# Kernel tuning notes

Hardware: AMD Instinct MI355X
Metric: run time of the kernel (lower is better)

## Reference

```python
import jax, jax.numpy as jnp
import numpy as np
import math

NUM_FILTERS = 128
SAMPLE_RATE = 16000
N_FFT = 2048
FREQ_MIN, FREQ_MAX = 20.0, 8000.0


def setup_inputs() -> dict:
    key = jax.random.key(0)
    B, FB, T = 32, N_FFT // 2 + 1, 2000
    spectrum = jax.random.normal(key, (B, FB, T), dtype=jnp.float32)
    # mel-scale init of center frequencies (in FFT-bin units), as in __init__
    mel_min = 2595.0 * math.log10(1.0 + FREQ_MIN / 700.0)
    mel_max = 2595.0 * math.log10(1.0 + FREQ_MAX / 700.0)
    mel_points = jnp.linspace(mel_min, mel_max, NUM_FILTERS, dtype=jnp.float32)
    freq_points = 700.0 * (10.0 ** (mel_points / 2595.0) - 1.0)
    center_freqs = freq_points * N_FFT / SAMPLE_RATE  # [F]
    bandwidths = jnp.full((NUM_FILTERS,), N_FFT / NUM_FILTERS / 4.0, dtype=jnp.float32)
    filter_shapes = jnp.ones((NUM_FILTERS, 2), dtype=jnp.float32)
    return {"spectrum": spectrum, "center_freqs": center_freqs,
            "bandwidths": bandwidths, "filter_shapes": filter_shapes}


def _build_filterbank(center_freqs, bandwidths, filter_shapes, freq_bins):
    # Vectorized over all filters: [F, freq_bins]
    freqs = jnp.arange(freq_bins, dtype=jnp.float32)[None, :]        # [1, K]
    center = center_freqs[:, None]                                    # [F, 1]
    bw = (jax.nn.softplus(bandwidths) + 0.001)[:, None]               # [F, 1]
    slopes = jax.nn.softplus(filter_shapes) + 0.1                     # [F, 2]
    left_edge = center - bw * slopes[:, 0:1]
    right_edge = center + bw * slopes[:, 1:2]
    rise = (freqs >= left_edge) & (freqs <= center)
    fall = (freqs > center) & (freqs <= right_edge)
    resp = jnp.where(rise, (freqs - left_edge) / (center - left_edge + 1e-8), 0.0)
    resp = jnp.where(fall, 1.0 - (freqs - center) / (right_edge - center + 1e-8), resp)
    return resp  # [F, K]


def reference(spectrum, center_freqs, bandwidths, filter_shapes):
    B, K, T = spectrum.shape
    F = center_freqs.shape[0]
    filterbank = _build_filterbank(center_freqs, bandwidths, filter_shapes, K)
    # [F, K] x [B, K, T] -> [B, F, T]
    filtered = jnp.einsum('fk,bkt->bft', filterbank, spectrum)
    # Faithful to original: reshape [B, F, T] -> [F, B, T], then permute(1,2,0) -> [B, T, F]
    filtered = filtered.reshape(F, B, T)
    return jnp.transpose(filtered, (1, 2, 0))
```

## Files before the change

kernel.cpp:

```cpp
#include <hip/hip_runtime.h>

#define K_BINS 1025
#define T_LEN  2000
#define NF     128
#define TQ     500
#define ROWQ   500
#define SLICE  524

__device__ __forceinline__ float softplusf(float x) {
    return fmaxf(x, 0.0f) + log1pf(expf(-fabsf(x)));
}

__global__ __launch_bounds__(1024) void fb_fused(
        const float* __restrict__ spec,
        const float* __restrict__ cf,
        const float* __restrict__ bwv,
        const float* __restrict__ fs,
        float*       __restrict__ out) {
    __shared__ float tile2[16][4 * SLICE];

    const int q    = blockIdx.x;
    const int B    = blockIdx.y;
    const int th   = blockIdx.z;
    const int tid  = threadIdx.x;
    const int lane = tid & 63;
    const int wid  = tid >> 6;
    const int w    = wid >> 2;
    const int p    = wid & 3;
    const int bp   = 4 * q + p;
    const int t0   = TQ * th;
    const bool ok1 = lane < (TQ / 4 - 64);
    const int  li1 = min(64 + lane, TQ / 4 - 1);

    const float4* base4 =
        (const float4*)(spec + (size_t)bp * (K_BINS * (size_t)T_LEN) + t0);

    float ic[4], mir[4], mA[4], Bfc[4];
    int   klo4[4], khi4[4];
#pragma unroll
    for (int i = 0; i < 4; ++i) {
        const int f = 4 * B + 32 * w + i;
        float c  = cf[f];
        float bw = softplusf(bwv[f]) + 0.001f;
        float s0 = softplusf(fs[2 * f])     + 0.1f;
        float s1 = softplusf(fs[2 * f + 1]) + 0.1f;
        float left  = c - bw * s0;
        float right = c + bw * s1;
        float icv = 1.0f / (c - left + 1e-8f);
        float irv = 1.0f / (right - c + 1e-8f);
        ic[i]  = icv;
        mir[i] = -irv;
        mA[i]  = -left * icv;
        Bfc[i] = fmaf(c, irv, 1.0f);
        klo4[i] = max(0, (int)ceilf(left));
        khi4[i] = min(K_BINS - 1, (int)floorf(right));
    }

    int RS0 = klo4[0], RE0 = khi4[0];
    int RS1 = 0, RE1 = -1, RS2 = 0, RE2 = -1, RS3 = 0, RE3 = -1;
    int nr = 1;
#pragma unroll
    for (int i = 1; i < 4; ++i) {
        const int s = klo4[i], e = khi4[i];
        const int le = (nr == 1) ? RE0 : (nr == 2) ? RE1 : RE2;
        if (s <= le + 1) {
            const int ne = max(le, e);
            if (nr == 1) RE0 = ne; else if (nr == 2) RE1 = ne; else RE2 = ne;
        } else {
            if (nr == 1)      { RS1 = s; RE1 = e; }
            else if (nr == 2) { RS2 = s; RE2 = e; }
            else              { RS3 = s; RE3 = e; }
            ++nr;
        }
    }

    float4 acc[4][2];
#pragma unroll
    for (int i = 0; i < 4; ++i) {
        acc[i][0] = make_float4(0.f, 0.f, 0.f, 0.f);
        acc[i][1] = make_float4(0.f, 0.f, 0.f, 0.f);
    }

#define ROWSTEP(KK, VA, VB)                                                 \
    { const int   k_  = (KK);                                               \
      const float fk_ = (float)k_;                                          \
      const bool  lv_ = (k_ <= ke);      \
      _Pragma("unroll")                                                     \
      for (int i = 0; i < 4; ++i) {                                         \
          float wg = fmaxf(0.0f, fminf(fmaf(fk_, ic[i],  mA[i]),            \
                                       fmaf(fk_, mir[i], Bfc[i])));         \
          wg = lv_ ? wg : 0.0f;                                             \
          acc[i][0].x = fmaf(wg, VA.x, acc[i][0].x);                        \
          acc[i][0].y = fmaf(wg, VA.y, acc[i][0].y);                        \
          acc[i][0].z = fmaf(wg, VA.z, acc[i][0].z);                        \
          acc[i][0].w = fmaf(wg, VA.w, acc[i][0].w);                        \
          acc[i][1].x = fmaf(wg, VB.x, acc[i][1].x);                        \
          acc[i][1].y = fmaf(wg, VB.y, acc[i][1].y);                        \
          acc[i][1].z = fmaf(wg, VB.z, acc[i][1].z);                        \
          acc[i][1].w = fmaf(wg, VB.w, acc[i][1].w);                        \
      } }

#pragma unroll
    for (int r = 0; r < 4; ++r) {
        int ks, ke;
        if      (r == 0) { ks = RS0; ke = RE0; }
        else if (r == 1) { ks = RS1; ke = RE1; }
        else if (r == 2) { ks = RS2; ke = RE2; }
        else             { ks = RS3; ke = RE3; }
        for (int k0 = ks; k0 <= ke; k0 += 4) {
            const float4* rp0 = base4 + (size_t)min(k0,     K_BINS - 1) * ROWQ;
            const float4* rp1 = base4 + (size_t)min(k0 + 1, K_BINS - 1) * ROWQ;
            const float4* rp2 = base4 + (size_t)min(k0 + 2, K_BINS - 1) * ROWQ;
            const float4* rp3 = base4 + (size_t)min(k0 + 3, K_BINS - 1) * ROWQ;
            float4 a0 = rp0[lane], b0 = rp0[li1];
            float4 a1 = rp1[lane], b1 = rp1[li1];
            float4 a2 = rp2[lane], b2 = rp2[li1];
            float4 a3 = rp3[lane], b3 = rp3[li1];
            ROWSTEP(k0 + 0, a0, b0);
            ROWSTEP(k0 + 1, a1, b1);
            ROWSTEP(k0 + 2, a2, b2);
            ROWSTEP(k0 + 3, a3, b3);
        }
    }
#undef ROWSTEP

    {
        const int col = 4 * p + w;
#pragma unroll
        for (int i = 0; i < 4; ++i) {
            *reinterpret_cast<float4*>(&tile2[col][i * SLICE + 4 * lane]) = acc[i][0];
            if (ok1)
                *reinterpret_cast<float4*>(&tile2[col][i * SLICE + 256 + 4 * lane]) = acc[i][1];
        }
    }
    __syncthreads();
    {
        const int c4 = tid & 3;
#pragma unroll
        for (int i = 0; i < 4; ++i) {
            const int b2 = 4 * B + i;
#pragma unroll
            for (int rr = 0; rr < 2; ++rr) {
                int tl = 256 * rr + (tid >> 2);
                if (tl < TQ) {
                    float4 v = make_float4(tile2[4 * c4 + 0][i * SLICE + tl],
                                           tile2[4 * c4 + 1][i * SLICE + tl],
                                           tile2[4 * c4 + 2][i * SLICE + tl],
                                           tile2[4 * c4 + 3][i * SLICE + tl]);
                    *reinterpret_cast<float4*>(
                        out + ((size_t)b2 * T_LEN + t0 + tl) * NF + 16 * q + 4 * c4) = v;
                }
            }
        }
    }
}

extern "C" void kernel_launch(void* const* d_in, const int* in_sizes, int n_in,
                              void* d_out, int out_size, void* d_ws, size_t ws_size,
                              hipStream_t stream) {
    const float* spec = (const float*)d_in[0];
    const float* cf   = (const float*)d_in[1];
    const float* bwv  = (const float*)d_in[2];
    const float* fs   = (const float*)d_in[3];
    float* out = (float*)d_out;

    fb_fused<<<dim3(8, 8, 4), 1024, 0, stream>>>(spec, cf, bwv, fs, out);
}
```

Measured before the change: 62.07 us.

## Widen per-thread time tile and reshape grid to 512-thread blocks

Each wave now covers a 1000-sample time span with four float4 accumulators per filter, instead of 500 samples with two. Blocks shrink to 512 threads and the grid becomes 8x2x16. The shared-memory transpose is staged one filter at a time through a smaller tile, adding extra barriers. The aim is to amortise the per-row filter-weight computation over more columns and to improve occupancy with smaller blocks, at the cost of higher register pressure from 64 accumulators.

```diff
diff --git a/kernel.cpp b/kernel.cpp
--- a/kernel.cpp
+++ b/kernel.cpp
@@ -3,34 +3,36 @@
 #define K_BINS 1025
 #define T_LEN  2000
 #define NF     128
-#define TQ     500
+#define TH     1000
+#define THQ    250
 #define ROWQ   500
-#define SLICE  524
 
 __device__ __forceinline__ float softplusf(float x) {
     return fmaxf(x, 0.0f) + log1pf(expf(-fabsf(x)));
 }
 
-__global__ __launch_bounds__(1024) void fb_fused(
+__global__ __launch_bounds__(512, 2) void fb_fused(
         const float* __restrict__ spec,
         const float* __restrict__ cf,
         const float* __restrict__ bwv,
         const float* __restrict__ fs,
         float*       __restrict__ out) {
-    __shared__ float tile2[16][4 * SLICE];
+    __shared__ __align__(16) float tile[8][1004];
 
     const int q    = blockIdx.x;
-    const int B    = blockIdx.y;
-    const int th   = blockIdx.z;
+    const int hp   = blockIdx.y;
+    const int B    = blockIdx.z >> 1;
+    const int th   = blockIdx.z & 1;
     const int tid  = threadIdx.x;
     const int lane = tid & 63;
     const int wid  = tid >> 6;
-    const int w    = wid >> 2;
-    const int p    = wid & 3;
-    const int bp   = 4 * q + p;
-    const int t0   = TQ * th;
-    const bool ok1 = lane < (TQ / 4 - 64);
-    const int  li1 = min(64 + lane, TQ / 4 - 1);
+    const int j    = wid >> 2;
+    const int s    = wid & 3;
+    const int w    = j ? (3 - s) : s;
+    const int bp   = 4 * q + 2 * hp + j;
+    const int t0   = TH * th;
+    const bool ok3 = lane < (THQ - 192);
+    const int  li3 = min(192 + lane, THQ - 1);
 
     const float4* base4 =
         (const float4*)(spec + (size_t)bp * (K_BINS * (size_t)T_LEN) + t0);
@@ -61,27 +63,26 @@
     int nr = 1;
 #pragma unroll
     for (int i = 1; i < 4; ++i) {
-        const int s = klo4[i], e = khi4[i];
+        const int ss = klo4[i], e = khi4[i];
         const int le = (nr == 1) ? RE0 : (nr == 2) ? RE1 : RE2;
-        if (s <= le + 1) {
+        if (ss <= le + 1) {
             const int ne = max(le, e);
             if (nr == 1) RE0 = ne; else if (nr == 2) RE1 = ne; else RE2 = ne;
         } else {
-            if (nr == 1)      { RS1 = s; RE1 = e; }
-            else if (nr == 2) { RS2 = s; RE2 = e; }
-            else              { RS3 = s; RE3 = e; }
+            if (nr == 1)      { RS1 = ss; RE1 = e; }
+            else if (nr == 2) { RS2 = ss; RE2 = e; }
+            else              { RS3 = ss; RE3 = e; }
             ++nr;
         }
     }
 
-    float4 acc[4][2];
+    float4 acc[4][4];
 #pragma unroll
-    for (int i = 0; i < 4; ++i) {
-        acc[i][0] = make_float4(0.f, 0.f, 0.f, 0.f);
-        acc[i][1] = make_float4(0.f, 0.f, 0.f, 0.f);
-    }
+    for (int i = 0; i < 4; ++i)
+#pragma unroll
+        for (int m = 0; m < 4; ++m) acc[i][m] = make_float4(0.f, 0.f, 0.f, 0.f);
 
-#define ROWSTEP(KK, VA, VB)                                                 \
+#define ROWSTEP(KK, V0, V1, V2, V3)                                         \
     { const int   k_  = (KK);                                               \
       const float fk_ = (float)k_;                                          \
       const bool  lv_ = (k_ <= ke);      \
@@ -90,14 +91,22 @@
           float wg = fmaxf(0.0f, fminf(fmaf(fk_, ic[i],  mA[i]),            \
                                        fmaf(fk_, mir[i], Bfc[i])));         \
           wg = lv_ ? wg : 0.0f;                                             \
-          acc[i][0].x = fmaf(wg, VA.x, acc[i][0].x);                        \
-          acc[i][0].y = fmaf(wg, VA.y, acc[i][0].y);                        \
-          acc[i][0].z = fmaf(wg, VA.z, acc[i][0].z);                        \
-          acc[i][0].w = fmaf(wg, VA.w, acc[i][0].w);                        \
-          acc[i][1].x = fmaf(wg, VB.x, acc[i][1].x);                        \
-          acc[i][1].y = fmaf(wg, VB.y, acc[i][1].y);                        \
-          acc[i][1].z = fmaf(wg, VB.z, acc[i][1].z);                        \
-          acc[i][1].w = fmaf(wg, VB.w, acc[i][1].w);                        \
+          acc[i][0].x = fmaf(wg, V0.x, acc[i][0].x);                        \
+          acc[i][0].y = fmaf(wg, V0.y, acc[i][0].y);                        \
+          acc[i][0].z = fmaf(wg, V0.z, acc[i][0].z);                        \
+          acc[i][0].w = fmaf(wg, V0.w, acc[i][0].w);                        \
+          acc[i][1].x = fmaf(wg, V1.x, acc[i][1].x);                        \
+          acc[i][1].y = fmaf(wg, V1.y, acc[i][1].y);                        \
+          acc[i][1].z = fmaf(wg, V1.z, acc[i][1].z);                        \
+          acc[i][1].w = fmaf(wg, V1.w, acc[i][1].w);                        \
+          acc[i][2].x = fmaf(wg, V2.x, acc[i][2].x);                        \
+          acc[i][2].y = fmaf(wg, V2.y, acc[i][2].y);                        \
+          acc[i][2].z = fmaf(wg, V2.z, acc[i][2].z);                        \
+          acc[i][2].w = fmaf(wg, V2.w, acc[i][2].w);                        \
+          acc[i][3].x = fmaf(wg, V3.x, acc[i][3].x);                        \
+          acc[i][3].y = fmaf(wg, V3.y, acc[i][3].y);                        \
+          acc[i][3].z = fmaf(wg, V3.z, acc[i][3].z);                        \
+          acc[i][3].w = fmaf(wg, V3.w, acc[i][3].w);                        \
       } }
 
 #pragma unroll
@@ -112,44 +121,39 @@
             const float4* rp1 = base4 + (size_t)min(k0 + 1, K_BINS - 1) * ROWQ;
             const float4* rp2 = base4 + (size_t)min(k0 + 2, K_BINS - 1) * ROWQ;
             const float4* rp3 = base4 + (size_t)min(k0 + 3, K_BINS - 1) * ROWQ;
-            float4 a0 = rp0[lane], b0 = rp0[li1];
-            float4 a1 = rp1[lane], b1 = rp1[li1];
-            float4 a2 = rp2[lane], b2 = rp2[li1];
-            float4 a3 = rp3[lane], b3 = rp3[li1];
-            ROWSTEP(k0 + 0, a0, b0);
-            ROWSTEP(k0 + 1, a1, b1);
-            ROWSTEP(k0 + 2, a2, b2);
-            ROWSTEP(k0 + 3, a3, b3);
+            float4 a00 = rp0[lane], a01 = rp0[64 + lane], a02 = rp0[128 + lane], a03 = rp0[li3];
+            float4 a10 = rp1[lane], a11 = rp1[64 + lane], a12 = rp1[128 + lane], a13 = rp1[li3];
+            float4 a20 = rp2[lane], a21 = rp2[64 + lane], a22 = rp2[128 + lane], a23 = rp2[li3];
+            float4 a30 = rp3[lane], a31 = rp3[64 + lane], a32 = rp3[128 + lane], a33 = rp3[li3];
+            ROWSTEP(k0 + 0, a00, a01, a02, a03);
+            ROWSTEP(k0 + 1, a10, a11, a12, a13);
+            ROWSTEP(k0 + 2, a20, a21, a22, a23);
+            ROWSTEP(k0 + 3, a30, a31, a32, a33);
         }
     }
 #undef ROWSTEP
 
-    {
-        const int col = 4 * p + w;
+    const int col = 4 * j + w;
 #pragma unroll
-        for (int i = 0; i < 4; ++i) {
-            *reinterpret_cast<float4*>(&tile2[col][i * SLICE + 4 * lane]) = acc[i][0];
-            if (ok1)
-                *reinterpret_cast<float4*>(&tile2[col][i * SLICE + 256 + 4 * lane]) = acc[i][1];
-        }
-    }
-    __syncthreads();
-    {
-        const int c4 = tid & 3;
+    for (int i = 0; i < 4; ++i) {
+        __syncthreads();
+        *reinterpret_cast<float4*>(&tile[col][4 * lane])       = acc[i][0];
+        *reinterpret_cast<float4*>(&tile[col][256 + 4 * lane]) = acc[i][1];
+        *reinterpret_cast<float4*>(&tile[col][512 + 4 * lane]) = acc[i][2];
+        if (ok3)
+            *reinterpret_cast<float4*>(&tile[col][768 + 4 * lane]) = acc[i][3];
+        __syncthreads();
+        const int b2 = 4 * B + i;
+        const int c4 = tid & 1;
 #pragma unroll
-        for (int i = 0; i < 4; ++i) {
-            const int b2 = 4 * B + i;
-#pragma unroll
-            for (int rr = 0; rr < 2; ++rr) {
-                int tl = 256 * rr + (tid >> 2);
-                if (tl < TQ) {
-                    float4 v = make_float4(tile2[4 * c4 + 0][i * SLICE + tl],
-                                           tile2[4 * c4 + 1][i * SLICE + tl],
-                                           tile2[4 * c4 + 2][i * SLICE + tl],
-                                           tile2[4 * c4 + 3][i * SLICE + tl]);
-                    *reinterpret_cast<float4*>(
-                        out + ((size_t)b2 * T_LEN + t0 + tl) * NF + 16 * q + 4 * c4) = v;
-                }
+        for (int rr = 0; rr < 4; ++rr) {
+            int tl = 256 * rr + (tid >> 1);
+            if (tl < TH) {
+                float4 v = make_float4(tile[4 * c4 + 0][tl], tile[4 * c4 + 1][tl],
+                                       tile[4 * c4 + 2][tl], tile[4 * c4 + 3][tl]);
+                *reinterpret_cast<float4*>(
+                    out + ((size_t)b2 * T_LEN + t0 + tl) * NF
+                        + 16 * q + 8 * hp + 4 * c4) = v;
             }
         }
     }
@@ -164,5 +168,5 @@
     const float* fs   = (const float*)d_in[3];
     float* out = (float*)d_out;
 
-    fb_fused<<<dim3(8, 8, 4), 1024, 0, stream>>>(spec, cf, bwv, fs, out);
+    fb_fused<<<dim3(8, 2, 16), 512, 0, stream>>>(spec, cf, bwv, fs, out);
 }
```

New measurement: 78.74 us. 26.9% more time.
